# Kernel optimization log

Measured on AMD Instinct MI355X. Metric: run time of the kernel, lower is better.

## Reference

```python
import jax, jax.numpy as jnp
import numpy as np

DEPTH = 4
HEADS = 8
DIM = 512
MLP = 2048
EPS = 1e-5


def layernorm(x, w, b):
    m = x.mean(-1, keepdims=True)
    v = x.var(-1, keepdims=True)
    return (x - m) * jax.lax.rsqrt(v + EPS) * w + b


def setup_inputs() -> dict:
    key = jax.random.key(0)
    ks = jax.random.split(key, 6)
    s = 0.02
    x = jax.random.normal(ks[0], (4, 2048, DIM), dtype=jnp.float32)
    return {
        "x": x,
        "ln1_w": jnp.ones((DEPTH, DIM), jnp.float32),
        "ln1_b": jnp.zeros((DEPTH, DIM), jnp.float32),
        "qkv_w": jax.random.normal(ks[1], (DEPTH, 3 * DIM, DIM), jnp.float32) * s,
        "proj_w": jax.random.normal(ks[2], (DEPTH, DIM, DIM), jnp.float32) * s,
        "proj_b": jnp.zeros((DEPTH, DIM), jnp.float32),
        "ln2_w": jnp.ones((DEPTH, DIM), jnp.float32),
        "ln2_b": jnp.zeros((DEPTH, DIM), jnp.float32),
        "fc1_w": jax.random.normal(ks[3], (DEPTH, MLP, DIM), jnp.float32) * s,
        "fc1_b": jnp.zeros((DEPTH, MLP), jnp.float32),
        "fc2_w": jax.random.normal(ks[4], (DEPTH, DIM, MLP), jnp.float32) * s,
        "fc2_b": jnp.zeros((DEPTH, DIM), jnp.float32),
    }


def reference(x, ln1_w, ln1_b, qkv_w, proj_w, proj_b, ln2_w, ln2_b, fc1_w, fc1_b, fc2_w, fc2_b):
    B, N, C = x.shape
    Dh = C // HEADS
    scale = Dh ** (-0.5)
    for i in range(DEPTH):
        # PreNorm attention block
        h = layernorm(x, ln1_w[i], ln1_b[i])
        qkv = (h @ qkv_w[i].T).reshape(B, N, 3, HEADS, Dh).transpose(2, 0, 3, 1, 4)
        q, k, v = qkv[0], qkv[1], qkv[2]          # [B,H,N,Dh]
        attn = jax.nn.softmax(jnp.einsum('bhnd,bhmd->bhnm', q, k) * scale, axis=-1)
        o = jnp.einsum('bhnm,bhmd->bhnd', attn, v).transpose(0, 2, 1, 3).reshape(B, N, C)
        x = o @ proj_w[i].T + proj_b[i] + x
        # PreNorm FFN block (exact erf GELU, matching torch nn.GELU default)
        h = layernorm(x, ln2_w[i], ln2_b[i])
        h = jax.nn.gelu(h @ fc1_w[i].T + fc1_b[i], approximate=False)
        x = h @ fc2_w[i].T + fc2_b[i] + x
    return x
```

## Files before the change

### kernel.cpp

```cpp
#include <hip/hip_runtime.h>
#include <hip/hip_bf16.h>
#include <math.h>

#define NB 4
#define HEADS 8
#define DIM 512
#define MLP 2048
#define NT 2048
#define DH 64
#define M_TOK (NB*NT)

typedef __bf16 bf16;
typedef __bf16 bf16x2 __attribute__((ext_vector_type(2)));
typedef __bf16 bf16x4 __attribute__((ext_vector_type(4)));
typedef __bf16 bf16x8 __attribute__((ext_vector_type(8)));
typedef float f32x4 __attribute__((ext_vector_type(4)));

__device__ __forceinline__ void gl_lds16(const void* g, void* l) {
    __builtin_amdgcn_global_load_lds((const __attribute__((address_space(1))) unsigned int*)g,
                                     (__attribute__((address_space(3))) unsigned int*)l, 16, 0, 0);
}

#define BARRIER() do { __builtin_amdgcn_s_barrier(); asm volatile("" ::: "memory"); } while(0)
#define WAIT_VM4() asm volatile("s_waitcnt vmcnt(4)" ::: "memory")
#define WAIT_VM0() asm volatile("s_waitcnt vmcnt(0)" ::: "memory")

__global__ void cvt_bf16_kernel(const float* __restrict__ src, bf16* __restrict__ dst, int n) {
    int i = (blockIdx.x * 256 + threadIdx.x) * 4;
    if (i < n) {
        float4 v = *(const float4*)(src + i);
        bf16x4 o;
        o[0] = (bf16)v.x; o[1] = (bf16)v.y; o[2] = (bf16)v.z; o[3] = (bf16)v.w;
        *(bf16x4*)(dst + i) = o;
    }
}

__global__ void ln_kernel(const float* __restrict__ X, const float* __restrict__ gam,
                          const float* __restrict__ bet, bf16* __restrict__ out) {
    int w = threadIdx.x >> 6, l = threadIdx.x & 63;
    long row = (long)blockIdx.x * 4 + w;
    const float* xp = X + row * DIM + l * 8;
    float4 a = *(const float4*)xp;
    float4 b = *(const float4*)(xp + 4);
    float s1 = a.x + a.y + a.z + a.w + b.x + b.y + b.z + b.w;
    float s2 = a.x*a.x + a.y*a.y + a.z*a.z + a.w*a.w + b.x*b.x + b.y*b.y + b.z*b.z + b.w*b.w;
#pragma unroll
    for (int off = 32; off; off >>= 1) { s1 += __shfl_xor(s1, off); s2 += __shfl_xor(s2, off); }
    float mean = s1 * (1.f / 512.f);
    float var  = s2 * (1.f / 512.f) - mean * mean;
    float rstd = rsqrtf(var + 1e-5f);
    float4 g0 = *(const float4*)(gam + l * 8), g1 = *(const float4*)(gam + l * 8 + 4);
    float4 b0 = *(const float4*)(bet + l * 8), b1 = *(const float4*)(bet + l * 8 + 4);
    bf16x8 o;
    o[0] = (bf16)((a.x - mean) * rstd * g0.x + b0.x);
    o[1] = (bf16)((a.y - mean) * rstd * g0.y + b0.y);
    o[2] = (bf16)((a.z - mean) * rstd * g0.z + b0.z);
    o[3] = (bf16)((a.w - mean) * rstd * g0.w + b0.w);
    o[4] = (bf16)((b.x - mean) * rstd * g1.x + b1.x);
    o[5] = (bf16)((b.y - mean) * rstd * g1.y + b1.y);
    o[6] = (bf16)((b.z - mean) * rstd * g1.z + b1.z);
    o[7] = (bf16)((b.w - mean) * rstd * g1.w + b1.w);
    *(bf16x8*)(out + row * DIM + l * 8) = o;
}

#define G_LOADA(AF, B_, MQ) do { \
  _Pragma("unroll") for (int mi_ = 0; mi_ < 2; ++mi_) \
  _Pragma("unroll") for (int kk_ = 0; kk_ < 2; ++kk_) { \
    int row_ = wr * 64 + ((MQ) * 2 + mi_) * 16 + c; \
    AF[mi_][kk_] = *(const bf16x8*)&Abuf[B_][row_ * 64 + (((kk_ * 64 + g * 16) ^ sw) >> 1)]; \
  } } while (0)

#define G_LOADB(BF, B_, NQ) do { \
  _Pragma("unroll") for (int ni_ = 0; ni_ < 2; ++ni_) \
  _Pragma("unroll") for (int kk_ = 0; kk_ < 2; ++kk_) { \
    int row_ = wc * 64 + ((NQ) * 2 + ni_) * 16 + c; \
    BF[ni_][kk_] = *(const bf16x8*)&Bbuf[B_][row_ * 64 + (((kk_ * 64 + g * 16) ^ sw) >> 1)]; \
  } } while (0)

#define G_MFMA(AF, BF, MQ, NQ) do { \
  __builtin_amdgcn_s_setprio(1); \
  _Pragma("unroll") for (int mi_ = 0; mi_ < 2; ++mi_) \
  _Pragma("unroll") for (int ni_ = 0; ni_ < 2; ++ni_) \
  _Pragma("unroll") for (int kk_ = 0; kk_ < 2; ++kk_) \
    acc[(MQ)*2+mi_][(NQ)*2+ni_] = __builtin_amdgcn_mfma_f32_16x16x32_bf16( \
        AF[mi_][kk_], BF[ni_][kk_], acc[(MQ)*2+mi_][(NQ)*2+ni_], 0, 0, 0); \
  __builtin_amdgcn_s_setprio(0); \
} while (0)

#define G_STAGE_A(J_, H_) do { int j_ = (J_); if (j_ < nkt) { \
  bf16* db_ = Abuf[j_ & 1]; const bf16* sb_ = Aptr + (size_t)j_ * 64 + coloff; \
  _Pragma("unroll") for (int q_ = 0; q_ < 2; ++q_) { \
    int rw_ = q_ * 64 + (H_) * 32 + (w << 3); \
    gl_lds16(sb_ + (size_t)(arow0 + rw_ + lr) * KN, db_ + rw_ * 64); \
  } } } while (0)

#define G_STAGE_B(J_, H_) do { int j_ = (J_); if (j_ < nkt) { \
  bf16* db_ = Bbuf[j_ & 1]; const bf16* sb_ = Wptr + (size_t)j_ * 64 + coloff; \
  _Pragma("unroll") for (int q_ = 0; q_ < 2; ++q_) { \
    int rw_ = q_ * 64 + (H_) * 32 + (w << 3); \
    gl_lds16(sb_ + (size_t)(bcol0 + rw_ + lr) * KN, db_ + rw_ * 64); \
  } } } while (0)

template<int EPI, int KN>
__global__ __launch_bounds__(256, 2) void gemm128(const bf16* __restrict__ Aptr,
                                                  const bf16* __restrict__ Wptr,
                                                  const float* __restrict__ bias,
                                                  const float* __restrict__ resid,
                                                  void* outp, int N, bf16* __restrict__ vtout) {
    __shared__ bf16 Abuf[2][128 * 64];
    __shared__ bf16 Bbuf[2][128 * 64];
    const int t = threadIdx.x, w = t >> 6, l = t & 63;
    const int wr = w >> 1, wc = w & 1, g = l >> 4, c = l & 15;
    const int sw = (c & 7) << 4;
    const int lr = l >> 3;
    const int coloff = ((l & 7) ^ lr) << 3;

    int nwg = gridDim.x, bid = blockIdx.x;
    int q8 = nwg >> 3, r8 = nwg & 7;
    int xcd = bid & 7, rank = bid >> 3;
    int swz = (xcd < r8) ? xcd * (q8 + 1) + rank : r8 * (q8 + 1) + (xcd - r8) * q8 + rank;
    int tiles_n = N >> 7;
    long arow0 = (long)(swz / tiles_n) * 128;
    long bcol0 = (long)(swz % tiles_n) * 128;

    const int nkt = KN / 64;
    const int niter = nkt / 2;
    f32x4 acc[4][4] = {};
    bf16x8 af[2][2], bn0[2][2], bn1[2][2];

    G_STAGE_A(0, 0); G_STAGE_B(0, 0); G_STAGE_A(0, 1); G_STAGE_B(0, 1);
    G_STAGE_A(1, 0); G_STAGE_B(1, 0);

#pragma unroll 1
    for (int tt = 0; tt < niter; ++tt) {
        const int J0 = 2 * tt, J1 = 2 * tt + 1;
        const bool last = (tt == niter - 1);
        WAIT_VM4(); BARRIER();
        G_LOADA(af, 0, 0); G_LOADB(bn0, 0, 0);
        G_STAGE_A(J0 + 1, 1);
        G_MFMA(af, bn0, 0, 0);
        BARRIER();
        G_LOADB(bn1, 0, 1);
        G_STAGE_B(J0 + 1, 1);
        G_MFMA(af, bn1, 0, 1);
        BARRIER();
        G_LOADA(af, 0, 1);
        G_STAGE_A(J0 + 2, 0);
        G_MFMA(af, bn0, 1, 0);
        BARRIER();
        G_STAGE_B(J0 + 2, 0);
        G_MFMA(af, bn1, 1, 1);
        BARRIER();
        if (last) { WAIT_VM0(); } else { WAIT_VM4(); }
        BARRIER();
        G_LOADA(af, 1, 0); G_LOADB(bn0, 1, 0);
        G_STAGE_A(J1 + 1, 1);
        G_MFMA(af, bn0, 0, 0);
        BARRIER();
        G_LOADB(bn1, 1, 1);
        G_STAGE_B(J1 + 1, 1);
        G_MFMA(af, bn1, 0, 1);
        BARRIER();
        G_LOADA(af, 1, 1);
        G_STAGE_A(J1 + 2, 0);
        G_MFMA(af, bn0, 1, 0);
        BARRIER();
        G_STAGE_B(J1 + 2, 0);
        G_MFMA(af, bn1, 1, 1);
        BARRIER();
    }

    if constexpr (EPI == 0) {
        const int s = (int)(bcol0 >> 9);
        if (s == 2) {
#pragma unroll
            for (int m = 0; m < 4; ++m)
#pragma unroll
                for (int n = 0; n < 4; ++n) {
                    int col = (int)(bcol0 + wc * 64 + n * 16 + c);
                    int d = col & 63, hh = (col >> 6) & 7;
                    long row = arow0 + wr * 64 + m * 16 + g * 4;
                    int bb = (int)(row >> 11), nn = (int)(row & 2047);
                    bf16x4 o4;
#pragma unroll
                    for (int r = 0; r < 4; ++r) o4[r] = (bf16)acc[m][n][r];
                    *(bf16x4*)(vtout + ((long)(bb * 8 + hh) * 64 + d) * 2048 + nn) = o4;
                }
        } else {
#pragma unroll
            for (int m = 0; m < 4; ++m)
#pragma unroll
                for (int n = 0; n < 4; ++n) {
                    int col = (int)(bcol0 + wc * 64 + n * 16 + c);
                    int hh = (col >> 6) & 7, d = col & 63;
                    long row = arow0 + wr * 64 + m * 16 + g * 4;
#pragma unroll
                    for (int r = 0; r < 4; ++r) {
                        long rr = row + r;
                        int bb = (int)(rr >> 11), nn = (int)(rr & 2047);
                        ((bf16*)outp)[(((long)(s * NB + bb) * HEADS + hh) * NT + nn) * DH + d] =
                            (bf16)acc[m][n][r];
                    }
                }
        }
    } else {
#pragma unroll
        for (int m = 0; m < 4; ++m)
#pragma unroll
            for (int n = 0; n < 4; ++n) {
                long row = arow0 + wr * 64 + m * 16 + g * 4;
                long col = bcol0 + wc * 64 + n * 16 + c;
#pragma unroll
                for (int r = 0; r < 4; ++r) {
                    float v = acc[m][n][r];
                    long rr = row + r;
                    float u = v + bias[col];
                    float ge = 0.5f * u * (1.f + erff(u * 0.70710678118654752f));
                    ((bf16*)outp)[rr * N + col] = (bf16)ge;
                }
            }
    }
}

template<int KN>
__global__ __launch_bounds__(256, 2) void gemm_n64(const bf16* __restrict__ A,
                                                   const bf16* __restrict__ W,
                                                   const float* __restrict__ bias,
                                                   const float* __restrict__ resid,
                                                   float* __restrict__ outp) {
    __shared__ bf16 As[128 * 64];
    __shared__ bf16 Bs[64 * 64];
    const int t = threadIdx.x, w = t >> 6, l = t & 63;
    const int wr = w >> 1, wc = w & 1, g = l >> 4, c = l & 15;
    const long arow0 = (long)blockIdx.y * 128;
    const long bcol0 = (long)blockIdx.x * 64;
    f32x4 acc[4][2] = {};
    const int lrow = l >> 3, lcol = (l & 7) * 8;
    const bf16* Ab = A + (arow0 + lrow) * (long)KN + lcol;
    const bf16* Wb = W + (bcol0 + lrow) * (long)KN + lcol;
    for (int k0 = 0; k0 < KN; k0 += 64) {
#pragma unroll
        for (int q = 0; q < 4; ++q)
            gl_lds16(Ab + (long)(w * 4 + q) * 8 * KN + k0, &As[(w * 4 + q) * 512]);
#pragma unroll
        for (int q = 0; q < 2; ++q)
            gl_lds16(Wb + (long)(w * 2 + q) * 8 * KN + k0, &Bs[(w * 2 + q) * 512]);
        __syncthreads();
#pragma unroll
        for (int kk = 0; kk < 2; ++kk) {
            bf16x8 afv[4], bfr[2];
#pragma unroll
            for (int m = 0; m < 4; ++m)
                afv[m] = *(const bf16x8*)&As[(wr * 64 + m * 16 + c) * 64 + kk * 32 + g * 8];
#pragma unroll
            for (int n = 0; n < 2; ++n)
                bfr[n] = *(const bf16x8*)&Bs[(wc * 32 + n * 16 + c) * 64 + kk * 32 + g * 8];
#pragma unroll
            for (int m = 0; m < 4; ++m)
#pragma unroll
                for (int n = 0; n < 2; ++n)
                    acc[m][n] = __builtin_amdgcn_mfma_f32_16x16x32_bf16(afv[m], bfr[n], acc[m][n], 0, 0, 0);
        }
        __syncthreads();
    }
#pragma unroll
    for (int m = 0; m < 4; ++m)
#pragma unroll
        for (int n = 0; n < 2; ++n) {
            long row = arow0 + wr * 64 + m * 16 + g * 4;
            long col = bcol0 + wc * 32 + n * 16 + c;
#pragma unroll
            for (int r = 0; r < 4; ++r) {
                long rr = row + r;
                outp[rr * 512 + col] = acc[m][n][r] + bias[col] + resid[rr * 512 + col];
            }
        }
}

#define NKT (NT / 64)

#define ATT_BODY(BUF, KT) do { \
    __syncthreads(); \
    if ((KT) + 1 < NKT) { \
        const bf16* ks_ = kbase + (size_t)((KT) + 1) * (64 * DH); \
        const bf16* vs_ = vbase + ((KT) + 1) * 64; \
        gl_lds16(ks_,           &Ks[(BUF) ^ 1][(w * 8) * 64]); \
        gl_lds16(ks_ + 32 * DH, &Ks[(BUF) ^ 1][(32 + w * 8) * 64]); \
        gl_lds16(vs_,           &Vs[(BUF) ^ 1][(w * 8) * 64]); \
        gl_lds16(vs_ + 32 * NT, &Vs[(BUF) ^ 1][(32 + w * 8) * 64]); \
    } \
    const bf16* ksb = &Ks[BUF][0]; \
    const char* vsb = (const char*)&Vs[BUF][0]; \
    bf16x8 kf[4][2]; \
    _Pragma("unroll") for (int kc = 0; kc < 4; ++kc) \
    _Pragma("unroll") for (int kk = 0; kk < 2; ++kk) \
        kf[kc][kk] = *(const bf16x8*)&ksb[(kc * 16 + c) * 64 + (((kk * 64 + g * 16) ^ xr) >> 1)]; \
    f32x4 st[4] = {}; \
    _Pragma("unroll") for (int kc = 0; kc < 4; ++kc) \
    _Pragma("unroll") for (int kk = 0; kk < 2; ++kk) \
        st[kc] = __builtin_amdgcn_mfma_f32_16x16x32_bf16(kf[kc][kk], qf[kk], st[kc], 0, 0, 0); \
    bf16x8 vf[4][2]; \
    _Pragma("unroll") for (int dc = 0; dc < 4; ++dc) \
    _Pragma("unroll") for (int ks = 0; ks < 2; ++ks) \
        vf[dc][ks] = *(const bf16x8*)(vsb + (dc * 16 + c) * 128 + ((ks * 64 + g * 16) ^ xr)); \
    float p[4][4]; \
    _Pragma("unroll") for (int a = 0; a < 4; ++a) \
    _Pragma("unroll") for (int r = 0; r < 4; ++r) { \
        float pv = exp2f(st[a][r] * cs); \
        p[a][r] = pv; lpart += pv; \
    } \
    bf16x8 pf[2]; \
    _Pragma("unroll") for (int ks = 0; ks < 2; ++ks) \
    _Pragma("unroll") for (int j = 0; j < 8; ++j) pf[ks][j] = (bf16)p[2 * ks + (j >> 2)][j & 3]; \
    _Pragma("unroll") for (int dc = 0; dc < 4; ++dc) \
    _Pragma("unroll") for (int ks = 0; ks < 2; ++ks) \
        oacc[dc] = __builtin_amdgcn_mfma_f32_16x16x32_bf16(vf[dc][ks], pf[ks], oacc[dc], 0, 0, 0); \
} while (0)

__global__ __launch_bounds__(256, 4) void attn_kernel(const bf16* __restrict__ qkv,
                                                      const bf16* __restrict__ vt,
                                                      bf16* __restrict__ O) {
    __shared__ bf16 Ks[2][64 * 64];
    __shared__ bf16 Vs[2][64 * 64];
    const int t = threadIdx.x, w = t >> 6, l = t & 63;
    const int g = l >> 4, c = l & 15;
    const int wg = blockIdx.x;
    const int xcd = wg & 7, rank = wg >> 3;
    const int bh = xcd + 8 * (rank >> 5);
    const int qt = rank & 31;
    const bf16* Qb = qkv + (long)bh * (NT * DH);
    const bf16* Kb = Qb + (long)(NB * HEADS) * (NT * DH);
    const bf16* Vtb = vt + (long)bh * (DH * NT);
    const int q0 = qt * 64 + w * 16;
    const int lr = l >> 3, lc = l & 7;
    const int sch = ((lc ^ lr) & 7) * 8;
    const int xr = (c & 7) << 4;
    const float cs = 0.18033688011112042f;

    const bf16* kbase = Kb + (long)(w * 8 + lr) * DH + sch;
    const bf16* vbase = Vtb + (long)(w * 8 + lr) * NT + sch;

    bf16x8 qf[2];
#pragma unroll
    for (int kk = 0; kk < 2; ++kk)
        qf[kk] = *(const bf16x8*)(Qb + (long)(q0 + c) * DH + kk * 32 + g * 8);

    f32x4 oacc[4] = {};
    float lpart = 0.f;

    gl_lds16(kbase,           &Ks[0][(w * 8) * 64]);
    gl_lds16(kbase + 32 * DH, &Ks[0][(32 + w * 8) * 64]);
    gl_lds16(vbase,           &Vs[0][(w * 8) * 64]);
    gl_lds16(vbase + 32 * NT, &Vs[0][(32 + w * 8) * 64]);

#pragma unroll 1
    for (int kt2 = 0; kt2 < NKT / 2; ++kt2) {
        ATT_BODY(0, kt2 * 2);
        ATT_BODY(1, kt2 * 2 + 1);
    }

    lpart += __shfl_xor(lpart, 16);
    lpart += __shfl_xor(lpart, 32);
    float inv = 1.f / lpart;

    char* ol = (char*)&Ks[0][0] + w * 2048;
#pragma unroll
    for (int dc = 0; dc < 4; ++dc) {
        bf16x4 o4;
#pragma unroll
        for (int r = 0; r < 4; ++r) o4[r] = (bf16)(oacc[dc][r] * inv);
        *(bf16x4*)(ol + c * 128 + ((dc * 32 + g * 8) ^ xr)) = o4;
    }
    const int orow = l >> 2, oc = (l & 3) * 16;
    const int bb = bh >> 3, hh = bh & 7;
    long tok = (long)bb * NT + q0 + orow;
    bf16* og = O + tok * DIM + hh * 64 + oc;
    const int xr2 = (orow & 7) << 4;
    bf16x8 v0 = *(const bf16x8*)(ol + orow * 128 + ((oc * 2) ^ xr2));
    bf16x8 v1 = *(const bf16x8*)(ol + orow * 128 + ((oc * 2 + 16) ^ xr2));
    *(bf16x8*)og = v0;
    *(bf16x8*)(og + 8) = v1;
}

extern "C" void kernel_launch(void* const* d_in, const int* in_sizes, int n_in,
                              void* d_out, int out_size, void* d_ws, size_t ws_size,
                              hipStream_t stream) {
    const float* x      = (const float*)d_in[0];
    const float* ln1_w  = (const float*)d_in[1];
    const float* ln1_b  = (const float*)d_in[2];
    const float* qkv_w  = (const float*)d_in[3];
    const float* proj_w = (const float*)d_in[4];
    const float* proj_b = (const float*)d_in[5];
    const float* ln2_w  = (const float*)d_in[6];
    const float* ln2_b  = (const float*)d_in[7];
    const float* fc1_w  = (const float*)d_in[8];
    const float* fc1_b  = (const float*)d_in[9];
    const float* fc2_w  = (const float*)d_in[10];
    const float* fc2_b  = (const float*)d_in[11];
    float* X = (float*)d_out;

    char* ws = (char*)d_ws;
    bf16* h_bf   = (bf16*)(ws);
    bf16* scr_bf = (bf16*)(ws + (size_t)(8  << 20));
    bf16* vt_bf  = (bf16*)(ws + (size_t)(32 << 20));
    bf16* o_bf   = (bf16*)(ws + (size_t)(40 << 20));
    bf16* w_qkv  = (bf16*)(ws + (size_t)(48 << 20));
    bf16* w_proj = w_qkv  + (size_t)4 * 1536 * 512;
    bf16* w_fc1  = w_proj + (size_t)4 * 512 * 512;
    bf16* w_fc2  = w_fc1  + (size_t)4 * 2048 * 512;

    {
        int n;
        n = 4 * 1536 * 512; cvt_bf16_kernel<<<n / 1024, 256, 0, stream>>>(qkv_w,  w_qkv,  n);
        n = 4 * 512 * 512;  cvt_bf16_kernel<<<n / 1024, 256, 0, stream>>>(proj_w, w_proj, n);
        n = 4 * 2048 * 512; cvt_bf16_kernel<<<n / 1024, 256, 0, stream>>>(fc1_w,  w_fc1,  n);
        n = 4 * 512 * 2048; cvt_bf16_kernel<<<n / 1024, 256, 0, stream>>>(fc2_w,  w_fc2,  n);
    }
    hipMemcpyAsync(X, x, (size_t)M_TOK * DIM * sizeof(float), hipMemcpyDeviceToDevice, stream);

    for (int i = 0; i < 4; ++i) {
        ln_kernel<<<M_TOK / 4, 256, 0, stream>>>(X, ln1_w + i * 512, ln1_b + i * 512, h_bf);
        gemm128<0, 512><<<(M_TOK / 128) * (1536 / 128), 256, 0, stream>>>(
            h_bf, w_qkv + (size_t)i * 1536 * 512, nullptr, nullptr, scr_bf, 1536, vt_bf);
        attn_kernel<<<1024, 256, 0, stream>>>(scr_bf, vt_bf, o_bf);
        gemm_n64<512><<<dim3(8, 64), 256, 0, stream>>>(
            o_bf, w_proj + (size_t)i * 512 * 512, proj_b + i * 512, X, X);
        ln_kernel<<<M_TOK / 4, 256, 0, stream>>>(X, ln2_w + i * 512, ln2_b + i * 512, h_bf);
        gemm128<2, 512><<<(M_TOK / 128) * (2048 / 128), 256, 0, stream>>>(
            h_bf, w_fc1 + (size_t)i * 2048 * 512, fc1_b + i * 2048, nullptr, scr_bf, 2048, nullptr);
        gemm_n64<2048><<<dim3(8, 64), 256, 0, stream>>>(
            scr_bf, w_fc2 + (size_t)i * 512 * 2048, fc2_b + i * 512, X, X);
    }
}
```

Measured before the change: 750.3 us.

## Prescale Q in QKV epilogue, use MFMA row-sum in attention, move fc1 to n64 GEMM

The QKV GEMM epilogue now multiplies Q by softmax scale times log2e, so the attention loop calls exp2f directly without a multiply. The softmax denominator is accumulated with an MFMA against a ones vector instead of scalar adds followed by cross-lane shuffles. Separately, fc1 with its GELU epilogue moves from the 128x128 gemm128 kernel to the templated 128x64 gemm_n64 kernel, and the gemm128 GELU path is removed. Extra MFMAs and the smaller fc1 tile with less reuse may offset the savings. The row sum now uses bf16-rounded probabilities.

```diff
diff --git a/kernel.cpp b/kernel.cpp
--- a/kernel.cpp
+++ b/kernel.cpp
@@ -172,6 +172,7 @@
 
     if constexpr (EPI == 0) {
         const int s = (int)(bcol0 >> 9);
+        const float qscale = 0.18033688011112042f;
         if (s == 2) {
 #pragma unroll
             for (int m = 0; m < 4; ++m)
@@ -187,6 +188,7 @@
                     *(bf16x4*)(vtout + ((long)(bb * 8 + hh) * 64 + d) * 2048 + nn) = o4;
                 }
         } else {
+            const float sc = (s == 0) ? qscale : 1.0f;
 #pragma unroll
             for (int m = 0; m < 4; ++m)
 #pragma unroll
@@ -199,35 +201,19 @@
                         long rr = row + r;
                         int bb = (int)(rr >> 11), nn = (int)(rr & 2047);
                         ((bf16*)outp)[(((long)(s * NB + bb) * HEADS + hh) * NT + nn) * DH + d] =
-                            (bf16)acc[m][n][r];
+                            (bf16)(acc[m][n][r] * sc);
                     }
                 }
         }
-    } else {
-#pragma unroll
-        for (int m = 0; m < 4; ++m)
-#pragma unroll
-            for (int n = 0; n < 4; ++n) {
-                long row = arow0 + wr * 64 + m * 16 + g * 4;
-                long col = bcol0 + wc * 64 + n * 16 + c;
-#pragma unroll
-                for (int r = 0; r < 4; ++r) {
-                    float v = acc[m][n][r];
-                    long rr = row + r;
-                    float u = v + bias[col];
-                    float ge = 0.5f * u * (1.f + erff(u * 0.70710678118654752f));
-                    ((bf16*)outp)[rr * N + col] = (bf16)ge;
-                }
-            }
-    }
-}
-
-template<int KN>
+    }
+}
+
+template<int KN, int NOUT, int EPI>
 __global__ __launch_bounds__(256, 2) void gemm_n64(const bf16* __restrict__ A,
                                                    const bf16* __restrict__ W,
                                                    const float* __restrict__ bias,
                                                    const float* __restrict__ resid,
-                                                   float* __restrict__ outp) {
+                                                   void* __restrict__ outp) {
     __shared__ bf16 As[128 * 64];
     __shared__ bf16 Bs[64 * 64];
     const int t = threadIdx.x, w = t >> 6, l = t & 63;
@@ -272,7 +258,13 @@
 #pragma unroll
             for (int r = 0; r < 4; ++r) {
                 long rr = row + r;
-                outp[rr * 512 + col] = acc[m][n][r] + bias[col] + resid[rr * 512 + col];
+                float v = acc[m][n][r] + bias[col];
+                if constexpr (EPI == 1) {
+                    ((float*)outp)[rr * NOUT + col] = v + resid[rr * NOUT + col];
+                } else {
+                    float ge = 0.5f * v * (1.f + erff(v * 0.70710678118654752f));
+                    ((bf16*)outp)[rr * NOUT + col] = (bf16)ge;
+                }
             }
         }
 }
@@ -303,15 +295,12 @@
     _Pragma("unroll") for (int dc = 0; dc < 4; ++dc) \
     _Pragma("unroll") for (int ks = 0; ks < 2; ++ks) \
         vf[dc][ks] = *(const bf16x8*)(vsb + (dc * 16 + c) * 128 + ((ks * 64 + g * 16) ^ xr)); \
-    float p[4][4]; \
+    bf16x8 pf[2]; \
     _Pragma("unroll") for (int a = 0; a < 4; ++a) \
-    _Pragma("unroll") for (int r = 0; r < 4; ++r) { \
-        float pv = exp2f(st[a][r] * cs); \
-        p[a][r] = pv; lpart += pv; \
-    } \
-    bf16x8 pf[2]; \
+    _Pragma("unroll") for (int r = 0; r < 4; ++r) \
+        pf[a >> 1][(a & 1) * 4 + r] = (bf16)exp2f(st[a][r]); \
     _Pragma("unroll") for (int ks = 0; ks < 2; ++ks) \
-    _Pragma("unroll") for (int j = 0; j < 8; ++j) pf[ks][j] = (bf16)p[2 * ks + (j >> 2)][j & 3]; \
+        sacc = __builtin_amdgcn_mfma_f32_16x16x32_bf16(ones8, pf[ks], sacc, 0, 0, 0); \
     _Pragma("unroll") for (int dc = 0; dc < 4; ++dc) \
     _Pragma("unroll") for (int ks = 0; ks < 2; ++ks) \
         oacc[dc] = __builtin_amdgcn_mfma_f32_16x16x32_bf16(vf[dc][ks], pf[ks], oacc[dc], 0, 0, 0); \
@@ -335,7 +324,6 @@
     const int lr = l >> 3, lc = l & 7;
     const int sch = ((lc ^ lr) & 7) * 8;
     const int xr = (c & 7) << 4;
-    const float cs = 0.18033688011112042f;
 
     const bf16* kbase = Kb + (long)(w * 8 + lr) * DH + sch;
     const bf16* vbase = Vtb + (long)(w * 8 + lr) * NT + sch;
@@ -345,8 +333,12 @@
     for (int kk = 0; kk < 2; ++kk)
         qf[kk] = *(const bf16x8*)(Qb + (long)(q0 + c) * DH + kk * 32 + g * 8);
 
+    bf16x8 ones8;
+#pragma unroll
+    for (int j = 0; j < 8; ++j) ones8[j] = (bf16)1.0f;
+
     f32x4 oacc[4] = {};
-    float lpart = 0.f;
+    f32x4 sacc = {};
 
     gl_lds16(kbase,           &Ks[0][(w * 8) * 64]);
     gl_lds16(kbase + 32 * DH, &Ks[0][(32 + w * 8) * 64]);
@@ -359,9 +351,7 @@
         ATT_BODY(1, kt2 * 2 + 1);
     }
 
-    lpart += __shfl_xor(lpart, 16);
-    lpart += __shfl_xor(lpart, 32);
-    float inv = 1.f / lpart;
+    float inv = 1.f / sacc[0];
 
     char* ol = (char*)&Ks[0][0] + w * 2048;
 #pragma unroll
@@ -423,12 +413,12 @@
         gemm128<0, 512><<<(M_TOK / 128) * (1536 / 128), 256, 0, stream>>>(
             h_bf, w_qkv + (size_t)i * 1536 * 512, nullptr, nullptr, scr_bf, 1536, vt_bf);
         attn_kernel<<<1024, 256, 0, stream>>>(scr_bf, vt_bf, o_bf);
-        gemm_n64<512><<<dim3(8, 64), 256, 0, stream>>>(
+        gemm_n64<512, 512, 1><<<dim3(8, 64), 256, 0, stream>>>(
             o_bf, w_proj + (size_t)i * 512 * 512, proj_b + i * 512, X, X);
         ln_kernel<<<M_TOK / 4, 256, 0, stream>>>(X, ln2_w + i * 512, ln2_b + i * 512, h_bf);
-        gemm128<2, 512><<<(M_TOK / 128) * (2048 / 128), 256, 0, stream>>>(
-            h_bf, w_fc1 + (size_t)i * 2048 * 512, fc1_b + i * 2048, nullptr, scr_bf, 2048, nullptr);
-        gemm_n64<2048><<<dim3(8, 64), 256, 0, stream>>>(
+        gemm_n64<512, 2048, 2><<<dim3(32, 64), 256, 0, stream>>>(
+            h_bf, w_fc1 + (size_t)i * 2048 * 512, fc1_b + i * 2048, nullptr, scr_bf);
+        gemm_n64<2048, 512, 1><<<dim3(8, 64), 256, 0, stream>>>(
             scr_bf, w_fc2 + (size_t)i * 512 * 2048, fc2_b + i * 512, X, X);
     }
 }
```

Result: no change. 743.0 us (-1.0%).
